# Optimization experiments

Measured on AMD Instinct MI355X. Metric: run time of the kernel, lower is better.

The kernel has to match this reference:

```python
import jax, jax.numpy as jnp
import numpy as np

N = 1048576
HID = 256
GEO = 15
POS_LAT = 3 + 10 * 2 * 3  # 63
DIR_LAT = 3 + 4 * 2 * 3   # 27
AABB_MIN = -1.5
AABB_MAX = 1.5


def sinus_enc(x, min_deg, max_deg):
    # x: [..., 3] -> [..., 3 + (max_deg-min_deg)*2*3] (identity + sin/cos bands)
    scales = 2.0 ** jnp.arange(min_deg, max_deg, dtype=x.dtype)
    xb = (x[..., None, :] * scales[:, None]).reshape(
        x.shape[:-1] + ((max_deg - min_deg) * x.shape[-1],))
    latent = jnp.sin(jnp.concatenate([xb, xb + 0.5 * np.pi], axis=-1))
    return jnp.concatenate([x, latent], axis=-1)


def trunc_exp(x):
    return jnp.exp(x)


def setup_inputs() -> dict:
    key = jax.random.key(0)
    ks = jax.random.split(key, 12)
    positions = jax.random.uniform(ks[0], (N, 3), dtype=jnp.float32,
                                   minval=AABB_MIN, maxval=AABB_MAX)
    directions = jax.random.normal(ks[1], (N, 3), dtype=jnp.float32)
    s = 0.05
    return {
        "positions": positions,
        "directions": directions,
        "W1": jax.random.normal(ks[2], (POS_LAT, HID), jnp.float32) * s,
        "b1": jnp.zeros((HID,), jnp.float32),
        "W2": jax.random.normal(ks[3], (HID, HID), jnp.float32) * s,
        "b2": jnp.zeros((HID,), jnp.float32),
        "W3": jax.random.normal(ks[4], (HID, HID), jnp.float32) * s,
        "b3": jnp.zeros((HID,), jnp.float32),
        "W4": jax.random.normal(ks[5], (HID, 1 + GEO), jnp.float32) * s,
        "b4": jnp.zeros((1 + GEO,), jnp.float32),
        "Wc1": jax.random.normal(ks[6], (GEO + DIR_LAT, HID // 2), jnp.float32) * s,
        "bc1": jnp.zeros((HID // 2,), jnp.float32),
        "Wc2": jax.random.normal(ks[7], (HID // 2, 3), jnp.float32) * s,
        "bc2": jnp.zeros((3,), jnp.float32),
    }


def reference(positions, directions, W1, b1, W2, b2, W3, b3, W4, b4,
              Wc1, bc1, Wc2, bc2):
    # normalize positions into [-1, 1] within the aabb
    x = (positions - AABB_MIN) / (AABB_MAX - AABB_MIN) * 2.0 - 1.0
    pe = sinus_enc(x, 0, 10)  # [N, 63]
    h = jax.nn.relu(pe @ W1 + b1)
    h = jax.nn.relu(h @ W2 + b2)
    h = jax.nn.relu(h @ W3 + b3)
    h = h @ W4 + b4  # [N, 16]
    density = trunc_exp(h[..., 0:1] - 1.0)  # [N, 1]
    feat = h[..., 1:]  # [N, 15]

    nrm = jnp.linalg.norm(directions, axis=-1, keepdims=True)
    d = directions / jnp.maximum(nrm, 1e-12)
    de = sinus_enc(d, 0, 4)  # [N, 27]
    hc = jnp.concatenate([feat, de], axis=-1)  # [N, 42]
    hc = jax.nn.relu(hc @ Wc1 + bc1)
    rgb = jax.nn.sigmoid(hc @ Wc2 + bc2)  # [N, 3]
    return rgb, density
```

## Files before the change

kernel.cpp:

```cpp
#include <hip/hip_runtime.h>

typedef unsigned short u16;
typedef __attribute__((ext_vector_type(8))) short short8;
typedef __attribute__((ext_vector_type(4))) float f32x4;
typedef __attribute__((ext_vector_type(16))) float f32x16;
typedef __attribute__((ext_vector_type(2))) unsigned int u32x2;

#define NPTS 1048576
#define TILES 128
#define NBLK (NPTS / (32 * TILES))
#define HPE 72
#define HPB 264
#define HPF 136

__device__ __forceinline__ u16 f2b(float f) {
    return (u16)((__float_as_uint(f) + 0x8000u) >> 16);
}
#define INV2PI 0.15915494309189535f
__device__ __forceinline__ float sinrev(float t) {
    t = t - floorf(t);
    return __builtin_amdgcn_sinf(t);
}

__global__ void prep_weights(const float* __restrict__ W1, const float* __restrict__ b1,
                             const float* __restrict__ W2,
                             const float* __restrict__ W3, const float* __restrict__ W4,
                             const float* __restrict__ Wc1, const float* __restrict__ bc1,
                             const float* __restrict__ Wc2,
                             u16* __restrict__ ws) {
    int i = blockIdx.x * 256 + threadIdx.x;
    if (i < 16384) { int n = i >> 6, k = i & 63;  ws[i]          = (k < 63) ? f2b(W1[k * 256 + n]) : f2b(b1[n]); return; }
    i -= 16384;
    if (i < 65536) { int n = i >> 8, k = i & 255; ws[16384 + i]  = f2b(W2[k * 256 + n]); return; }
    i -= 65536;
    if (i < 65536) { int n = i >> 8, k = i & 255; ws[81920 + i]  = f2b(W3[k * 256 + n]); return; }
    i -= 65536;
    if (i < 4096)  { int n = i >> 8, k = i & 255; ws[147456 + i] = f2b(W4[k * 16 + n]); return; }
    i -= 4096;
    if (i < 8192)  { int n = i >> 6, k = i & 63;
                     ws[151552 + i] = (k < 42) ? f2b(Wc1[k * 128 + n]) : ((k == 42) ? f2b(bc1[n]) : (u16)0); return; }
    i -= 8192;
    if (i < 2048)  { int n = i >> 7, k = i & 127; ws[159744 + i] = (n < 3) ? f2b(Wc2[k * 3 + n]) : (u16)0; return; }
}

template <bool BIAS>
__device__ __forceinline__ void epi32(const f32x16& acc, u16* rowp, const float* bias,
                                      int nbase, int kh) {
#pragma unroll
    for (int g = 0; g < 4; ++g) {
        const int mq = nbase + 8 * g + 4 * kh;
        float v[4];
#pragma unroll
        for (int j = 0; j < 4; ++j) v[j] = acc[4 * g + j];
        if (BIAS) {
            const f32x4 bi = *(const f32x4*)(bias + mq);
#pragma unroll
            for (int j = 0; j < 4; ++j) v[j] += bi[j];
        }
#pragma unroll
        for (int j = 0; j < 4; ++j) v[j] = fmaxf(v[j], 0.f);
        unsigned int u[4];
#pragma unroll
        for (int j = 0; j < 4; ++j) u[j] = __float_as_uint(v[j]) + 0x8000u;
        u32x2 d;
        d.x = __builtin_amdgcn_perm(u[1], u[0], 0x07060302);
        d.y = __builtin_amdgcn_perm(u[3], u[2], 0x07060302);
        *(u32x2*)(rowp + mq) = d;
    }
}

template <int NKT, bool BIAS>
__device__ __forceinline__ void layer32(const short8* wr, const u16* src, int ss,
                                        u16* dst, int ds, const float* bias,
                                        int nbase, int ln, int kh) {
    f32x16 acc;
#pragma unroll
    for (int r = 0; r < 16; ++r) acc[r] = 0.f;
#pragma unroll
    for (int kt = 0; kt < NKT; ++kt) {
        const short8 bA = *(const short8*)(src + ln * ss + kt * 16 + kh * 8);
        acc = __builtin_amdgcn_mfma_f32_32x32x16_bf16(wr[kt], bA, acc, 0, 0, 0);
    }
    epi32<BIAS>(acc, dst + ln * ds, bias, nbase, kh);
}

__device__ __forceinline__ void enc_preload(const float* __restrict__ pos,
                                            const float* __restrict__ dir,
                                            long rb, int j, float* v) {
    if (j < 256) {
        const long row = rb + (j >> 3);
        v[0] = pos[row * 3 + 0]; v[1] = pos[row * 3 + 1]; v[2] = pos[row * 3 + 2];
    } else {
        const long row = rb + ((j - 256) >> 3);
        v[0] = dir[row * 3 + 0]; v[1] = dir[row * 3 + 1]; v[2] = dir[row * 3 + 2];
    }
}

__device__ __forceinline__ void enc_compute(const float* v, int j, u16* sEj, u16* sGj) {
    if (j < 256) {
        const int r = j >> 3, g = j & 7;
        float xn[3];
#pragma unroll
        for (int c = 0; c < 3; ++c) xn[c] = v[c] * (1.0f / 1.5f);
        u16* er = sEj + r * HPE;
        if (g < 5) {
#pragma unroll
            for (int dd = 0; dd < 2; ++dd) {
                const int d = 2 * g + dd;
                const float sc = (float)(1 << d);
#pragma unroll
                for (int c = 0; c < 3; ++c) {
                    float tv = xn[c] * sc * INV2PI;
                    er[3 + d * 3 + c]  = f2b(sinrev(tv));
                    er[33 + d * 3 + c] = f2b(sinrev(tv + 0.25f));
                }
            }
        } else if (g == 5) {
            er[0] = f2b(xn[0]); er[1] = f2b(xn[1]); er[2] = f2b(xn[2]);
            er[63] = 0x3F80;
        }
    } else {
        const int j2 = j - 256;
        const int r = j2 >> 3, g = j2 & 7;
        u16* gr = sGj + r * HPE;
        const float dx = v[0], dy = v[1], dz = v[2];
        if (g < 6) {
            const float nrm = sqrtf(dx * dx + dy * dy + dz * dz);
            const float inv = 1.f / fmaxf(nrm, 1e-12f);
            const float dn[3] = {dx * inv, dy * inv, dz * inv};
            if (g < 4) {
                const float sc = (float)(1 << g);
#pragma unroll
                for (int c = 0; c < 3; ++c) {
                    float tv = dn[c] * sc * INV2PI;
                    gr[18 + g * 3 + c] = f2b(sinrev(tv));
                    gr[30 + g * 3 + c] = f2b(sinrev(tv + 0.25f));
                }
            } else if (g == 4) {
                gr[15] = f2b(dn[0]); gr[16] = f2b(dn[1]); gr[17] = f2b(dn[2]);
            } else {
                gr[42] = 0x3F80;
#pragma unroll
                for (int c = 43; c < 50; ++c) gr[c] = 0;
            }
        } else if (g == 6) {
#pragma unroll
            for (int c = 50; c < 57; ++c) gr[c] = 0;
        } else {
#pragma unroll
            for (int c = 57; c < 64; ++c) gr[c] = 0;
        }
    }
}

__global__ __launch_bounds__(1024, 4) void ngp_fused(
    const float* __restrict__ pos, const float* __restrict__ dir, const u16* __restrict__ ws,
    const float* __restrict__ b2, const float* __restrict__ b3,
    const float* __restrict__ b4, const float* __restrict__ bc2,
    float* __restrict__ out) {
    __shared__ __align__(16) u16 sE[2][32][HPE];
    __shared__ __align__(16) u16 sB[2][32][HPB];
    __shared__ __align__(16) u16 sC[2][32][HPB];
    __shared__ __align__(16) u16 sD[2][32][HPB];
    __shared__ __align__(16) u16 sG[6][32][HPE];
    __shared__ __align__(16) u16 sF[2][32][HPF];
    const int t = threadIdx.x;
    const int lane = t & 63;
    const int w = t >> 6;
    const int bw = w - 8;
    const int ln = lane & 31, kh = lane >> 5;
    const int lr = lane & 15, q = lane >> 4;

    const u16* WT1  = ws;
    const u16* WT2  = ws + 16384;
    const u16* WT3  = ws + 81920;
    const u16* WT4  = ws + 147456;
    const u16* WTc1 = ws + 151552;
    const u16* WTc2 = ws + 159744;

    short8 wrA[16], wrB[4];
    {
        const u16* pA = (w < 8) ? WT2 + (size_t)(w * 32 + ln) * 256 + kh * 8
                                : WT3 + (size_t)(bw * 32 + ln) * 256 + kh * 8;
#pragma unroll
        for (int kt = 0; kt < 16; ++kt) wrA[kt] = *(const short8*)(pA + kt * 16);
        const u16* pB = (w < 8)  ? WT1 + (size_t)(w * 32 + ln) * 64 + kh * 8
                      : (bw < 4) ? WTc1 + (size_t)(bw * 32 + ln) * 64 + kh * 8
                                 : WT1 + (size_t)ln * 64 + kh * 8;
#pragma unroll
        for (int kt = 0; kt < 4; ++kt) wrB[kt] = *(const short8*)(pB + kt * 16);
    }

    {
        float pv[3];
        if (t >= 512) {
            enc_preload(pos, dir, (long)blockIdx.x * TILES * 32, t - 512, pv);
            enc_compute(pv, t - 512, &sE[0][0][0], &sG[0][0][0]);
        }
        __syncthreads();
    }

    int gE = 1;
    for (int i = 0; i <= TILES + 4; ++i) {
        const bool dEnc = (i + 1 < TILES);
        const bool dL1  = (i < TILES);
        const bool dL2  = (i >= 1 && i <= TILES);
        const bool dL3  = (i >= 2 && i <= TILES + 1);
        const bool dL4  = (i >= 3 && i <= TILES + 2);
        const bool dC1  = (i >= 4 && i <= TILES + 3);
        const bool dHd  = (i >= 5);
        int gF = gE + 2; if (gF >= 6) gF -= 6;
        int gC = gE + 1; if (gC >= 6) gC -= 6;

        if (w < 8) {
            if (dL2)
                layer32<16, true>(wrA, &sB[(i - 1) & 1][0][0], HPB, &sC[(i - 1) & 1][0][0], HPB,
                                  b2, w * 32, ln, kh);
            if (dL1)
                layer32<4, false>(wrB, &sE[i & 1][0][0], HPE, &sB[i & 1][0][0], HPB,
                                  nullptr, w * 32, ln, kh);
        } else {
            float pv[3];
            if (dEnc)
                enc_preload(pos, dir, ((long)blockIdx.x * TILES + i + 1) * 32, t - 512, pv);
            if (dL3)
                layer32<16, true>(wrA, &sC[(i - 2) & 1][0][0], HPB, &sD[(i - 2) & 1][0][0], HPB,
                                  b3, bw * 32, ln, kh);
            if (dL4 && (bw == 4 || bw == 5)) {
                const long rbM = ((long)blockIdx.x * TILES + i - 3) * 32;
                u16* sGf = &sG[gF][0][0];
                const int rbase = (bw - 4) * 16;
                f32x4 acc = {0.f, 0.f, 0.f, 0.f};
#pragma unroll
                for (int kt = 0; kt < 8; ++kt) {
                    const short8 aF = *(const short8*)&sD[(i - 3) & 1][rbase + lr][kt * 32 + q * 8];
                    const short8 bF = *(const short8*)(WT4 + lr * 256 + kt * 32 + q * 8);
                    acc = __builtin_amdgcn_mfma_f32_16x16x32_bf16(aF, bF, acc, 0, 0, 0);
                }
                const float bi = b4[lr];
#pragma unroll
                for (int r = 0; r < 4; ++r) {
                    const float v = acc[r] + bi;
                    const int gm = rbase + q * 4 + r;
                    if (lr == 0)
                        out[3 * (long)NPTS + rbM + gm] = __expf(v - 1.f);
                    else
                        sGf[gm * HPE + lr - 1] = f2b(v);
                }
            }
            if (dC1 && bw < 4)
                layer32<4, false>(wrB, &sG[gC][0][0], HPE, &sF[(i - 4) & 1][0][0], HPF,
                                  nullptr, bw * 32, ln, kh);
            if (dHd && (bw == 6 || bw == 7)) {
                const long rbH = ((long)blockIdx.x * TILES + i - 5) * 32;
                const int rbase = (bw - 6) * 16;
                f32x4 acc = {0.f, 0.f, 0.f, 0.f};
#pragma unroll
                for (int kt = 0; kt < 4; ++kt) {
                    const short8 aF = *(const short8*)&sF[(i - 5) & 1][rbase + lr][kt * 32 + q * 8];
                    const short8 bF = *(const short8*)(WTc2 + lr * 128 + kt * 32 + q * 8);
                    acc = __builtin_amdgcn_mfma_f32_16x16x32_bf16(aF, bF, acc, 0, 0, 0);
                }
                if (lr < 3) {
                    const float bi = bc2[lr];
#pragma unroll
                    for (int r = 0; r < 4; ++r) {
                        const float v = acc[r] + bi;
                        const float sg = 1.f / (1.f + __expf(-v));
                        out[(rbH + rbase + q * 4 + r) * 3 + lr] = sg;
                    }
                }
            }
            if (dEnc)
                enc_compute(pv, t - 512, &sE[(i + 1) & 1][0][0], &sG[gE][0][0]);
        }
        __syncthreads();
        gE = (gE + 1 == 6) ? 0 : gE + 1;
    }
}

extern "C" void kernel_launch(void* const* d_in, const int* in_sizes, int n_in,
                              void* d_out, int out_size, void* d_ws, size_t ws_size,
                              hipStream_t stream) {
    const float* pos = (const float*)d_in[0];
    const float* dir = (const float*)d_in[1];
    const float* W1  = (const float*)d_in[2];
    const float* b1  = (const float*)d_in[3];
    const float* W2  = (const float*)d_in[4];
    const float* b2  = (const float*)d_in[5];
    const float* W3  = (const float*)d_in[6];
    const float* b3  = (const float*)d_in[7];
    const float* W4  = (const float*)d_in[8];
    const float* b4  = (const float*)d_in[9];
    const float* Wc1 = (const float*)d_in[10];
    const float* bc1 = (const float*)d_in[11];
    const float* Wc2 = (const float*)d_in[12];
    const float* bc2 = (const float*)d_in[13];
    u16* ws   = (u16*)d_ws;
    float* out = (float*)d_out;

    prep_weights<<<633, 256, 0, stream>>>(W1, b1, W2, W3, W4, Wc1, bc1, Wc2, ws);
    ngp_fused<<<NBLK, 1024, 0, stream>>>(pos, dir, ws, b2, b3, b4, bc2, out);
}
```

Baseline: 594.8 us.

## Rebalance warp-specialized pipeline: split each iteration into two phases, add MFMA priority

Restructures the software pipeline so the first eight waves do encoding, layer 1 and then layer 2 of the same tile across two barrier-separated phases. The other eight waves split layer 3 across both phases and run layer 4 and the color head in the second phase. This shortens the pipeline by one stage, drops the sB and sG ring depth, and moves encoding work onto the first wave group. s_setprio is raised around MFMA loops to favour matrix-issuing waves. The cost is an extra __syncthreads per iteration and a different load balance between the two wave groups.

Measured after the change: 827.6 us. +39.1%, slower.

```diff
diff --git a/kernel.cpp b/kernel.cpp
--- a/kernel.cpp
+++ b/kernel.cpp
@@ -76,11 +76,13 @@
     f32x16 acc;
 #pragma unroll
     for (int r = 0; r < 16; ++r) acc[r] = 0.f;
+    __builtin_amdgcn_s_setprio(1);
 #pragma unroll
     for (int kt = 0; kt < NKT; ++kt) {
         const short8 bA = *(const short8*)(src + ln * ss + kt * 16 + kh * 8);
         acc = __builtin_amdgcn_mfma_f32_32x32x16_bf16(wr[kt], bA, acc, 0, 0, 0);
     }
+    __builtin_amdgcn_s_setprio(0);
     epi32<BIAS>(acc, dst + ln * ds, bias, nbase, kh);
 }
 
@@ -159,10 +161,10 @@
     const float* __restrict__ b4, const float* __restrict__ bc2,
     float* __restrict__ out) {
     __shared__ __align__(16) u16 sE[2][32][HPE];
-    __shared__ __align__(16) u16 sB[2][32][HPB];
+    __shared__ __align__(16) u16 sB[32][HPB];
     __shared__ __align__(16) u16 sC[2][32][HPB];
     __shared__ __align__(16) u16 sD[2][32][HPB];
-    __shared__ __align__(16) u16 sG[6][32][HPE];
+    __shared__ __align__(16) u16 sG[5][32][HPE];
     __shared__ __align__(16) u16 sF[2][32][HPF];
     const int t = threadIdx.x;
     const int lane = t & 63;
@@ -193,50 +195,77 @@
 
     {
         float pv[3];
-        if (t >= 512) {
-            enc_preload(pos, dir, (long)blockIdx.x * TILES * 32, t - 512, pv);
-            enc_compute(pv, t - 512, &sE[0][0][0], &sG[0][0][0]);
+        if (t < 512) {
+            enc_preload(pos, dir, (long)blockIdx.x * TILES * 32, t, pv);
+            enc_compute(pv, t, &sE[0][0][0], &sG[0][0][0]);
         }
         __syncthreads();
     }
 
     int gE = 1;
-    for (int i = 0; i <= TILES + 4; ++i) {
+    for (int i = 0; i <= TILES + 3; ++i) {
         const bool dEnc = (i + 1 < TILES);
         const bool dL1  = (i < TILES);
-        const bool dL2  = (i >= 1 && i <= TILES);
-        const bool dL3  = (i >= 2 && i <= TILES + 1);
-        const bool dL4  = (i >= 3 && i <= TILES + 2);
-        const bool dC1  = (i >= 4 && i <= TILES + 3);
-        const bool dHd  = (i >= 5);
-        int gF = gE + 2; if (gF >= 6) gF -= 6;
-        int gC = gE + 1; if (gC >= 6) gC -= 6;
+        const bool dL3  = (i >= 1 && i <= TILES);
+        const bool dL4  = (i >= 2 && i <= TILES + 1);
+        const bool dC1  = (i >= 3 && i <= TILES + 2);
+        const bool dHd  = (i >= 4);
+        int gF = gE + 2; if (gF >= 5) gF -= 5;
+        int gC = gE + 1; if (gC >= 5) gC -= 5;
+
+        f32x16 acc3;
+        const u16* srcC = &sC[(i - 1) & 1][0][0] + ln * HPB + kh * 8;
 
         if (w < 8) {
-            if (dL2)
-                layer32<16, true>(wrA, &sB[(i - 1) & 1][0][0], HPB, &sC[(i - 1) & 1][0][0], HPB,
-                                  b2, w * 32, ln, kh);
-            if (dL1)
-                layer32<4, false>(wrB, &sE[i & 1][0][0], HPE, &sB[i & 1][0][0], HPB,
-                                  nullptr, w * 32, ln, kh);
-        } else {
             float pv[3];
             if (dEnc)
-                enc_preload(pos, dir, ((long)blockIdx.x * TILES + i + 1) * 32, t - 512, pv);
-            if (dL3)
-                layer32<16, true>(wrA, &sC[(i - 2) & 1][0][0], HPB, &sD[(i - 2) & 1][0][0], HPB,
-                                  b3, bw * 32, ln, kh);
+                enc_preload(pos, dir, ((long)blockIdx.x * TILES + i + 1) * 32, t, pv);
+            if (dL1)
+                layer32<4, false>(wrB, &sE[i & 1][0][0], HPE, &sB[0][0], HPB,
+                                  nullptr, w * 32, ln, kh);
+            if (dEnc)
+                enc_compute(pv, t, &sE[(i + 1) & 1][0][0], &sG[gE][0][0]);
+        } else if (dL3) {
+#pragma unroll
+            for (int r = 0; r < 16; ++r) acc3[r] = 0.f;
+            __builtin_amdgcn_s_setprio(1);
+#pragma unroll
+            for (int kt = 0; kt < 8; ++kt) {
+                const short8 bA = *(const short8*)(srcC + kt * 16);
+                acc3 = __builtin_amdgcn_mfma_f32_32x32x16_bf16(wrA[kt], bA, acc3, 0, 0, 0);
+            }
+            __builtin_amdgcn_s_setprio(0);
+        }
+        __syncthreads();
+
+        if (w < 8) {
+            if (dL1)
+                layer32<16, true>(wrA, &sB[0][0], HPB, &sC[i & 1][0][0], HPB,
+                                  b2, w * 32, ln, kh);
+        } else {
+            if (dL3) {
+                __builtin_amdgcn_s_setprio(1);
+#pragma unroll
+                for (int kt = 8; kt < 16; ++kt) {
+                    const short8 bA = *(const short8*)(srcC + kt * 16);
+                    acc3 = __builtin_amdgcn_mfma_f32_32x32x16_bf16(wrA[kt], bA, acc3, 0, 0, 0);
+                }
+                __builtin_amdgcn_s_setprio(0);
+                epi32<true>(acc3, &sD[(i - 1) & 1][0][0] + ln * HPB, b3, bw * 32, kh);
+            }
             if (dL4 && (bw == 4 || bw == 5)) {
-                const long rbM = ((long)blockIdx.x * TILES + i - 3) * 32;
+                const long rbM = ((long)blockIdx.x * TILES + i - 2) * 32;
                 u16* sGf = &sG[gF][0][0];
                 const int rbase = (bw - 4) * 16;
                 f32x4 acc = {0.f, 0.f, 0.f, 0.f};
+                __builtin_amdgcn_s_setprio(1);
 #pragma unroll
                 for (int kt = 0; kt < 8; ++kt) {
-                    const short8 aF = *(const short8*)&sD[(i - 3) & 1][rbase + lr][kt * 32 + q * 8];
+                    const short8 aF = *(const short8*)&sD[(i - 2) & 1][rbase + lr][kt * 32 + q * 8];
                     const short8 bF = *(const short8*)(WT4 + lr * 256 + kt * 32 + q * 8);
                     acc = __builtin_amdgcn_mfma_f32_16x16x32_bf16(aF, bF, acc, 0, 0, 0);
                 }
+                __builtin_amdgcn_s_setprio(0);
                 const float bi = b4[lr];
 #pragma unroll
                 for (int r = 0; r < 4; ++r) {
@@ -249,18 +278,20 @@
                 }
             }
             if (dC1 && bw < 4)
-                layer32<4, false>(wrB, &sG[gC][0][0], HPE, &sF[(i - 4) & 1][0][0], HPF,
+                layer32<4, false>(wrB, &sG[gC][0][0], HPE, &sF[(i - 3) & 1][0][0], HPF,
                                   nullptr, bw * 32, ln, kh);
             if (dHd && (bw == 6 || bw == 7)) {
-                const long rbH = ((long)blockIdx.x * TILES + i - 5) * 32;
+                const long rbH = ((long)blockIdx.x * TILES + i - 4) * 32;
                 const int rbase = (bw - 6) * 16;
                 f32x4 acc = {0.f, 0.f, 0.f, 0.f};
+                __builtin_amdgcn_s_setprio(1);
 #pragma unroll
                 for (int kt = 0; kt < 4; ++kt) {
-                    const short8 aF = *(const short8*)&sF[(i - 5) & 1][rbase + lr][kt * 32 + q * 8];
+                    const short8 aF = *(const short8*)&sF[(i - 4) & 1][rbase + lr][kt * 32 + q * 8];
                     const short8 bF = *(const short8*)(WTc2 + lr * 128 + kt * 32 + q * 8);
                     acc = __builtin_amdgcn_mfma_f32_16x16x32_bf16(aF, bF, acc, 0, 0, 0);
                 }
+                __builtin_amdgcn_s_setprio(0);
                 if (lr < 3) {
                     const float bi = bc2[lr];
 #pragma unroll
@@ -271,11 +302,9 @@
                     }
                 }
             }
-            if (dEnc)
-                enc_compute(pv, t - 512, &sE[(i + 1) & 1][0][0], &sG[gE][0][0]);
         }
         __syncthreads();
-        gE = (gE + 1 == 6) ? 0 : gE + 1;
+        gE = (gE + 1 == 5) ? 0 : gE + 1;
     }
 }
 
```
